# Performance work log

Measured on AMD Instinct MI355X. Metric: run time of the kernel, lower is better.

## Reference

```python
import jax, jax.numpy as jnp
import numpy as np

N = 10000      # nodes
E = 80000      # edges (avg degree 8)
G = 64         # graphs in batch
HID = 256
RBF_K = 16
DEPTH = 6
KA, KC, KE = 16, 6, 5
DE = HID // 3          # 85, per-modality embedding dim
CAT = 3 * HID + RBF_K  # 784, width of [h_i, h_j, rbf, e_emb]
CUTOFF = 10.0


def _gumbel_hard(probs, noise, tau=1.0):
    """F.gumbel_softmax(log(probs), tau, hard=True) with externally supplied gumbel noise."""
    logits = jnp.log(jnp.clip(probs, 1e-12))
    y = jax.nn.softmax((logits + noise) / tau, axis=-1)
    hard = jax.nn.one_hot(jnp.argmax(y, axis=-1), y.shape[-1], dtype=y.dtype)
    return hard + y - jax.lax.stop_gradient(y)  # straight-through


def setup_inputs() -> dict:
    key = jax.random.key(0)
    ks = iter(jax.random.split(key, 80))

    def nrm(shape, fan):
        return jax.random.normal(next(ks), shape, jnp.float32) / np.sqrt(fan).astype(np.float32)

    def gumbel(shape):
        u = jax.random.uniform(next(ks), shape, minval=1e-9, maxval=1.0 - 1e-9)
        return -jnp.log(-jnp.log(u))

    inp = {}
    inp['a_t'] = jax.random.uniform(next(ks), (N, KA))
    inp['c_t'] = jax.random.uniform(next(ks), (N, KC))
    inp['e_t'] = jax.random.uniform(next(ks), (E, KE))
    inp['x_t'] = jax.random.normal(next(ks), (N, 3))
    inp['g_a'] = gumbel((N, KA))
    inp['g_c'] = gumbel((N, KC))
    inp['g_e'] = gumbel((E, KE))

    # embeddings / fuse / lift
    inp['atom_W'] = nrm((KA, DE), KA)
    inp['charge_W'] = nrm((KC, DE), KC)
    inp['bond_W'] = nrm((KE, DE), KE)
    inp['fuse_W'] = nrm((3 * DE, HID), 3 * DE)
    inp['fuse_b'] = jnp.zeros((HID,))
    inp['lift_W'] = nrm((DE, HID), DE)
    inp['lift_b'] = jnp.zeros((HID,))

    # stacked block params (DEPTH blocks)
    inp['phim_W1'] = nrm((DEPTH, CAT, HID), CAT)
    inp['phim_b1'] = jnp.zeros((DEPTH, HID))
    inp['phim_W2'] = nrm((DEPTH, HID, HID), HID)
    inp['phim_b2'] = jnp.zeros((DEPTH, HID))
    inp['phix_W1'] = nrm((DEPTH, HID, HID), HID)
    inp['phix_b1'] = jnp.zeros((DEPTH, HID))
    inp['phix_W2'] = nrm((DEPTH, HID, 1), HID)
    inp['phix_b2'] = jnp.zeros((DEPTH, 1))
    inp['psim_W1'] = nrm((DEPTH, CAT, HID), CAT)
    inp['psim_b1'] = jnp.zeros((DEPTH, HID))
    inp['psim_W2'] = nrm((DEPTH, HID, HID), HID)
    inp['psim_b2'] = jnp.zeros((DEPTH, HID))
    inp['updh_W1'] = nrm((DEPTH, 2 * HID, HID), 2 * HID)
    inp['updh_b1'] = jnp.zeros((DEPTH, HID))
    inp['updh_W2'] = nrm((DEPTH, HID, HID), HID)
    inp['updh_b2'] = jnp.zeros((DEPTH, HID))
    inp['ln_g'] = jnp.ones((DEPTH, HID))
    inp['ln_b'] = jnp.zeros((DEPTH, HID))
    inp['head_W'] = nrm((HID, 1), HID)
    inp['head_b'] = jnp.zeros((1,))

    inp['src'] = jax.random.randint(next(ks), (E,), 0, N)
    inp['dst'] = jax.random.randint(next(ks), (E,), 0, N)
    inp['node_graph'] = jnp.sort(jax.random.randint(next(ks), (N,), 0, G))
    return inp


def reference(a_t, c_t, e_t, x_t, g_a, g_c, g_e,
              atom_W, charge_W, bond_W, fuse_W, fuse_b, lift_W, lift_b,
              phim_W1, phim_b1, phim_W2, phim_b2,
              phix_W1, phix_b1, phix_W2, phix_b2,
              psim_W1, psim_b1, psim_W2, psim_b2,
              updh_W1, updh_b1, updh_W2, updh_b2,
              ln_g, ln_b, head_W, head_b,
              src, dst, node_graph):
    centers = jnp.linspace(0.0, CUTOFF, RBF_K)
    widths = jnp.full((RBF_K,), CUTOFF / RBF_K)

    # encode nodes: gumbel-hard embed atom & charge probs, zero x-slot, fuse
    a_h = _gumbel_hard(a_t, g_a) @ atom_W           # (N, DE)
    c_h = _gumbel_hard(c_t, g_c) @ charge_W         # (N, DE)
    h = jnp.concatenate([a_h, c_h, jnp.zeros_like(a_h)], axis=-1) @ fuse_W + fuse_b  # (N, HID)
    # encode edges
    e_emb = (_gumbel_hard(e_t, g_e) @ bond_W) @ lift_W + lift_b  # (E, HID)

    x = x_t
    for d in range(DEPTH):
        h_i, h_j = h[dst], h[src]                    # gather per edge
        rij = x[dst] - x[src]                        # (E, 3)
        dist = jnp.sqrt(jnp.clip(jnp.sum(rij * rij, -1, keepdims=True), 0.0))
        z = (dist - centers) / (widths + 1e-12)
        rbf = jnp.exp(-0.5 * z * z)                  # (E, RBF_K)
        cat = jnp.concatenate([h_i, h_j, rbf, e_emb], axis=-1)  # (E, 784)
        m = jax.nn.silu(jax.nn.silu(cat @ phim_W1[d] + phim_b1[d]) @ phim_W2[d] + phim_b2[d])
        gate = jax.nn.silu(m @ phix_W1[d] + phix_b1[d]) @ phix_W2[d] + phix_b2[d]  # (E, 1)
        pm = jax.nn.silu(jax.nn.silu(cat @ psim_W1[d] + psim_b1[d]) @ psim_W2[d] + psim_b2[d])
        dx_sum = jax.ops.segment_sum(rij * gate, dst, num_segments=N)   # scatter to dst
        pm_sum = jax.ops.segment_sum(pm, dst, num_segments=N)
        x = x + dx_sum
        u = jax.nn.silu(jnp.concatenate([h, pm_sum], -1) @ updh_W1[d] + updh_b1[d]) @ updh_W2[d] + updh_b2[d]
        z2 = h + u
        mu = jnp.mean(z2, -1, keepdims=True)
        var = jnp.mean((z2 - mu) ** 2, -1, keepdims=True)
        h = (z2 - mu) / jnp.sqrt(var + 1e-5) * ln_g[d] + ln_b[d]

    # mean readout per graph
    cnt = jax.ops.segment_sum(jnp.ones((h.shape[0], 1), h.dtype), node_graph, num_segments=G)
    hg = jax.ops.segment_sum(h, node_graph, num_segments=G) / jnp.maximum(cnt, 1.0)
    out = jax.nn.sigmoid((hg @ head_W + head_b) / 2.0)  # property='score' -> sigmoid, tau=2
    return out
```

## Files before the change

kernel.cpp:

```cpp
#include <hip/hip_runtime.h>
#include <math.h>

#define NN   10000
#define NE   80000
#define NG   64
#define HID  256
#define RBFK 16
#define NDEP 6
#define KA   16
#define KC   6
#define KE   5
#define DE   85
#define CATW 784

typedef __attribute__((ext_vector_type(8))) short bf16x8;
typedef __attribute__((ext_vector_type(4))) float f32x4;
typedef __attribute__((ext_vector_type(2))) __bf16 bf16v2;

#if __has_builtin(__builtin_amdgcn_fdot2_f32_bf16)
#define HAVE_BF16_DOT2 1
#else
#define HAVE_BF16_DOT2 0
#endif

static __device__ __forceinline__ float silu_f(float v) {
  return __fdividef(v, 1.0f + __expf(-v));
}

static __device__ __forceinline__ unsigned short f2bf(float f) {
  union { float f; unsigned int u; } v; v.f = f;
  unsigned int r = v.u + 0x7fff + ((v.u >> 16) & 1);
  return (unsigned short)(r >> 16);
}
static __device__ __forceinline__ float bf2f(unsigned short h) {
  union { unsigned int u; float f; } v; v.u = ((unsigned int)h) << 16;
  return v.f;
}
static __device__ __forceinline__ bf16v2 u2bf2(unsigned int u) {
  union { unsigned int u; bf16v2 v; } x; x.u = u; return x.v;
}

static __device__ __forceinline__ void gload16(const void* g, void* l) {
  __builtin_amdgcn_global_load_lds((const __attribute__((address_space(1))) unsigned int*)g,
                                   (__attribute__((address_space(3))) unsigned int*)l, 16, 0, 0);
}

__global__ void convw_plain(const float* __restrict__ W, unsigned short* __restrict__ Wt, int K,
                            long long wt_dstride, int wt_rowoff) {
  __shared__ float T[32][65];
  int k0 = blockIdx.x * 32, n0 = blockIdx.y * 64, d = blockIdx.z;
  int tid = threadIdx.x;
  int nn = tid & 63, kr = tid >> 6;
  const float* Wd = W + (size_t)d * K * 256;
#pragma unroll
  for (int i = 0; i < 8; ++i) {
    int k = kr + i * 4;
    T[k][nn] = Wd[(size_t)(k0 + k) * 256 + n0 + nn];
  }
  __syncthreads();
  unsigned short* Wtd = Wt + (size_t)d * wt_dstride;
  int kk = tid & 31, nr = tid >> 5;
#pragma unroll
  for (int i = 0; i < 8; ++i) {
    int n = nr + i * 8;
    Wtd[(size_t)(wt_rowoff + n0 + n) * K + k0 + kk] = f2bf(T[kk][n]);
  }
}

__global__ void convw_nodeblk(const float* __restrict__ W, unsigned short* __restrict__ Wt,
                              int src_k0, int nt_base) {
  __shared__ float T[32][65];
  int k0 = blockIdx.x * 32, n0 = blockIdx.y * 64, d = blockIdx.z;
  int tid = threadIdx.x;
  int nn = tid & 63, kr = tid >> 6;
  const float* Wd = W + (size_t)d * CATW * 256;
#pragma unroll
  for (int i = 0; i < 8; ++i) {
    int k = kr + i * 4;
    T[k][nn] = Wd[(size_t)(src_k0 + k0 + k) * 256 + n0 + nn];
  }
  __syncthreads();
  unsigned short* Wtd = Wt + (size_t)d * 1024 * 256;
  int kk = tid & 31, nr = tid >> 5;
#pragma unroll
  for (int i = 0; i < 8; ++i) {
    int n = nr + i * 8;
    Wtd[(size_t)(nt_base + n0 + n) * 256 + k0 + kk] = f2bf(T[kk][n]);
  }
}

__global__ void convw_rbf(const float* __restrict__ phimW1, const float* __restrict__ psimW1,
                          unsigned short* __restrict__ wR) {
  int d = blockIdx.x, j = threadIdx.x;
  int jj = j & 255;
  const float* W = (j < 256) ? phimW1 : psimW1;
  for (int k = 0; k < 16; ++k)
    wR[((size_t)d * 16 + k) * 512 + j] = f2bf(W[(size_t)d * CATW * 256 + (size_t)(512 + k) * 256 + jj]);
}

__global__ void convw_rbf2(const float* __restrict__ phimW1, const float* __restrict__ psimW1,
                           unsigned int* __restrict__ wRp) {
  int d = blockIdx.x, j = threadIdx.x;
  int jj = j & 255;
  const float* W = (j < 256) ? phimW1 : psimW1;
  const float* base = W + (size_t)d * CATW * 256;
  for (int p = 0; p < 8; ++p) {
    unsigned int lo = f2bf(base[(size_t)(512 + 2*p) * 256 + jj]);
    unsigned int hi = f2bf(base[(size_t)(512 + 2*p + 1) * 256 + jj]);
    wRp[((size_t)d * 8 + p) * 512 + j] = lo | (hi << 16);
  }
}

__global__ void tables_kernel(const float* __restrict__ atom_W, const float* __restrict__ charge_W,
                              const float* __restrict__ bond_W, const float* __restrict__ fuse_W,
                              const float* __restrict__ fuse_b, const float* __restrict__ lift_W,
                              const float* __restrict__ lift_b,
                              float* __restrict__ tabA, float* __restrict__ tabC,
                              float* __restrict__ tabEf) {
  int r = blockIdx.x, k = threadIdx.x;
  if (r < KA) {
    float s = 0.f;
    for (int d = 0; d < DE; ++d) s += atom_W[r*DE + d] * fuse_W[d*HID + k];
    tabA[r*HID + k] = s + fuse_b[k];
  } else if (r < KA + KC) {
    int rr = r - KA;
    float s = 0.f;
    for (int d = 0; d < DE; ++d) s += charge_W[rr*DE + d] * fuse_W[(DE + d)*HID + k];
    tabC[rr*HID + k] = s;
  } else {
    int rr = r - KA - KC;
    float s = 0.f;
    for (int d = 0; d < DE; ++d) s += bond_W[rr*DE + d] * lift_W[d*HID + k];
    tabEf[rr*HID + k] = s + lift_b[k];
  }
}

__global__ void tabe1_kernel(const float* __restrict__ tabEf,
                             const float* __restrict__ phimW1, const float* __restrict__ phimb1,
                             const float* __restrict__ psimW1, const float* __restrict__ psimb1,
                             unsigned short* __restrict__ tabE1) {
  int r = blockIdx.x, d = blockIdx.y, j = threadIdx.x;
  const float* W = (j < 256) ? phimW1 : psimW1;
  const float* b = (j < 256) ? phimb1 : psimb1;
  int jj = j & 255;
  float s = b[d*256 + jj];
  for (int k = 0; k < 256; ++k)
    s += tabEf[r*256 + k] * W[(size_t)d*CATW*256 + (size_t)(528 + k)*256 + jj];
  tabE1[((size_t)d*5 + r)*512 + j] = f2bf(s);
}

__global__ void node_init_kernel(const float* __restrict__ a_t, const float* __restrict__ c_t,
                                 const float* __restrict__ g_a, const float* __restrict__ g_c,
                                 const float* __restrict__ x_t, const float* __restrict__ tabA,
                                 const float* __restrict__ tabC, float* __restrict__ h,
                                 unsigned short* __restrict__ hbf, float* __restrict__ x) {
  int n = blockIdx.x;
  __shared__ int s_ia, s_ic;
  if (threadIdx.x == 0) {
    float best = -1e30f; int bi = 0;
    for (int j = 0; j < KA; ++j) {
      float v = logf(fmaxf(a_t[n*KA + j], 1e-12f)) + g_a[n*KA + j];
      if (v > best) { best = v; bi = j; }
    }
    s_ia = bi;
  }
  if (threadIdx.x == 1) {
    float best = -1e30f; int bi = 0;
    for (int j = 0; j < KC; ++j) {
      float v = logf(fmaxf(c_t[n*KC + j], 1e-12f)) + g_c[n*KC + j];
      if (v > best) { best = v; bi = j; }
    }
    s_ic = bi;
  }
  __syncthreads();
  int k = threadIdx.x;
  float v = tabA[s_ia*HID + k] + tabC[s_ic*HID + k];
  h[n*HID + k] = v;
  hbf[n*HID + k] = f2bf(v);
  if (k < 3) x[n*3 + k] = x_t[n*3 + k];
}

__global__ void edge_init_kernel(const float* __restrict__ e_t, const float* __restrict__ g_e,
                                 int* __restrict__ ie) {
  int e = blockIdx.x * blockDim.x + threadIdx.x;
  if (e >= NE) return;
  float best = -1e30f; int bi = 0;
  for (int j = 0; j < KE; ++j) {
    float v = logf(fmaxf(e_t[e*KE + j], 1e-12f)) + g_e[e*KE + j];
    if (v > best) { best = v; bi = j; }
  }
  ie[e] = bi;
}

__global__ void hist_kernel(const int* __restrict__ dst, int* __restrict__ deg) {
  int e = blockIdx.x * 256 + threadIdx.x;
  if (e < NE) atomicAdd(&deg[dst[e]], 1);
}

__global__ void scan_kernel(const int* __restrict__ deg, int* __restrict__ rowstart,
                            int* __restrict__ cursor) {
  __shared__ int tmp[1024];
  int t = threadIdx.x;
  int base = t * 10;
  int local[10];
  int s = 0;
#pragma unroll
  for (int i = 0; i < 10; ++i) { local[i] = deg[base + i]; s += local[i]; }
  tmp[t] = s;
  __syncthreads();
  for (int off = 1; off < 1024; off <<= 1) {
    int v = (t >= off) ? tmp[t - off] : 0;
    __syncthreads();
    tmp[t] += v;
    __syncthreads();
  }
  int run = (t == 0) ? 0 : tmp[t - 1];
#pragma unroll
  for (int i = 0; i < 10; ++i) {
    rowstart[base + i] = run; cursor[base + i] = run; run += local[i];
  }
  if (t == 1023) rowstart[10240] = run;
}

__global__ void fill_kernel(const int* __restrict__ dst, int* __restrict__ cursor,
                            int* __restrict__ eids) {
  int e = blockIdx.x * 256 + threadIdx.x;
  if (e >= NE) return;
  int pos = atomicAdd(&cursor[dst[e]], 1);
  eids[pos] = e;
}

__global__ void sortrows_kernel(const int* __restrict__ rowstart, int* __restrict__ eids) {
  int n = blockIdx.x * 256 + threadIdx.x;
  if (n >= NN) return;
  int s = rowstart[n], e = rowstart[n + 1];
  for (int i = s + 1; i < e; ++i) {
    int v = eids[i]; int j = i - 1;
    while (j >= s && eids[j] > v) { eids[j + 1] = eids[j]; --j; }
    eids[j + 1] = v;
  }
}

__global__ void gbound_kernel(const int* __restrict__ ng, int* __restrict__ gstart) {
  int n = blockIdx.x * 256 + threadIdx.x;
  if (n >= NN) return;
  if (n == 0) {
    for (int g = 0; g <= ng[0]; ++g) gstart[g] = 0;
  } else {
    int a = ng[n-1], b = ng[n];
    for (int g = a + 1; g <= b; ++g) gstart[g] = n;
  }
  if (n == NN - 1) {
    for (int g = ng[n] + 1; g <= NG; ++g) gstart[g] = NN;
  }
}

__global__ __launch_bounds__(256) void combine2_kernel(
    const int* __restrict__ srcp, const int* __restrict__ dstp, const int* __restrict__ iep,
    const float* __restrict__ x,
    const unsigned short* __restrict__ P,
    const unsigned short* __restrict__ tabE1,
    const unsigned short* __restrict__ wR,
    const unsigned int* __restrict__ wRp,
    unsigned short* __restrict__ c1, unsigned short* __restrict__ ps1) {
  const int tid = threadIdx.x;
  const int lane = tid & 63;
  const int e = blockIdx.x * 4 + (tid >> 6);
  const int half = lane >> 5;
  const int c8 = (lane & 31) * 8;
  const int ds = dstp[e], sr = srcp[e], ib = iep[e];
  float r0 = x[ds*3+0] - x[sr*3+0];
  float r1 = x[ds*3+1] - x[sr*3+1];
  float r2 = x[ds*3+2] - x[sr*3+2];
  float dist = sqrtf(r0*r0 + r1*r1 + r2*r2);
  int klo = (int)(dist * 1.5f) - 3;
  klo = klo < 0 ? 0 : (klo > 8 ? 8 : klo);
  const unsigned short* Pb0 = P + (size_t)(half * 2) * NN * 256;
  const unsigned short* Pb1 = P + (size_t)(half * 2 + 1) * NN * 256;
  bf16x8 pa = *(const bf16x8*)&Pb0[(size_t)ds * 256 + c8];
  bf16x8 pb = *(const bf16x8*)&Pb1[(size_t)sr * 256 + c8];
  bf16x8 te = *(const bf16x8*)&tabE1[(size_t)ib * 512 + lane * 8];
  float zv[8];
#pragma unroll
  for (int j = 0; j < 8; ++j)
    zv[j] = bf2f((unsigned short)pa[j]) + bf2f((unsigned short)pb[j]) + bf2f((unsigned short)te[j]);
#if HAVE_BF16_DOT2
  int plo = klo >> 1;
  if (plo > 4) plo = 4;
#pragma unroll
  for (int pp = 0; pp < 4; ++pp) {
    int pr = plo + pp;
    float k0f = (float)(2 * pr);
    float z0 = (dist - 0.66666667f * k0f) * 1.6f;
    float z1 = (dist - 0.66666667f * (k0f + 1.0f)) * 1.6f;
    unsigned int rkp = (unsigned int)f2bf(__expf(-0.5f * z0 * z0)) |
                       ((unsigned int)f2bf(__expf(-0.5f * z1 * z1)) << 16);
    bf16v2 rv = u2bf2(rkp);
    const unsigned int* w8 = wRp + (size_t)pr * 512 + lane * 8;
    uint4 wa = *(const uint4*)w8;
    uint4 wb = *(const uint4*)(w8 + 4);
    zv[0] = __builtin_amdgcn_fdot2_f32_bf16(rv, u2bf2(wa.x), zv[0], false);
    zv[1] = __builtin_amdgcn_fdot2_f32_bf16(rv, u2bf2(wa.y), zv[1], false);
    zv[2] = __builtin_amdgcn_fdot2_f32_bf16(rv, u2bf2(wa.z), zv[2], false);
    zv[3] = __builtin_amdgcn_fdot2_f32_bf16(rv, u2bf2(wa.w), zv[3], false);
    zv[4] = __builtin_amdgcn_fdot2_f32_bf16(rv, u2bf2(wb.x), zv[4], false);
    zv[5] = __builtin_amdgcn_fdot2_f32_bf16(rv, u2bf2(wb.y), zv[5], false);
    zv[6] = __builtin_amdgcn_fdot2_f32_bf16(rv, u2bf2(wb.z), zv[6], false);
    zv[7] = __builtin_amdgcn_fdot2_f32_bf16(rv, u2bf2(wb.w), zv[7], false);
  }
#else
  (void)wRp;
#pragma unroll
  for (int kk = 0; kk < 8; ++kk) {
    int k = klo + kk;
    float z = (dist - 0.66666667f * (float)k) * 1.6f;
    float rk = __expf(-0.5f * z * z);
    bf16x8 wv = *(const bf16x8*)&wR[k * 512 + lane * 8];
#pragma unroll
    for (int j = 0; j < 8; ++j)
      zv[j] += rk * bf2f((unsigned short)wv[j]);
  }
#endif
  unsigned short ov[8];
#pragma unroll
  for (int j = 0; j < 8; ++j) ov[j] = f2bf(silu_f(zv[j]));
  unsigned short* outp = half ? ps1 : c1;
  *(uint4*)&outp[(size_t)e * 256 + c8] = *(uint4*)ov;
}

template<int MODE, bool SILU, bool GATE, bool LNOUT, bool SMALL>
__global__ __launch_bounds__(SMALL ? 256 : 512, 4) void mfma_gemm(
    const unsigned short* __restrict__ A, const unsigned short* __restrict__ A2,
    const unsigned short* __restrict__ Wt,
    const float* __restrict__ bias, const float* __restrict__ bias2,
    unsigned short* __restrict__ C, unsigned short* __restrict__ C2,
    int M, int Kp, int Msplit,
    const float* __restrict__ gw2, float* __restrict__ gout,
    float* __restrict__ hf, unsigned short* __restrict__ hb,
    const float* __restrict__ lng, const float* __restrict__ lnb) {
  constexpr int BM = SMALL ? 64 : 128;
  constexpr int BQ = SMALL ? 8 : 4;
  __shared__ unsigned short lds[SMALL ? 20480 : 24576];
  unsigned short* As = lds;
  unsigned short* Bs = lds + BM * 64;
  const int tid = threadIdx.x;
  const int bn = blockIdx.x * 256;
  const int bm = blockIdx.y * BM;
  const int lane = tid & 63;
  const int w = tid >> 6;
  const int wr = SMALL ? 0 : (w >> 2);
  const int wc = SMALL ? w : (w & 3);
  const int subrow = lane >> 3;
  const int kd = 8 * ((lane & 7) ^ subrow);

  const bool half2 = (MODE == 4) && (bm >= Msplit);
  const unsigned short* Wb = Wt + (half2 ? 256 * 256 : 0);

  unsigned int offB[BQ];
#pragma unroll
  for (int q = 0; q < BQ; ++q)
    offB[q] = (unsigned)(bn + w * (BQ * 8) + q * 8 + subrow) * (unsigned)Kp;

  unsigned int offA[2];
#pragma unroll
  for (int q = 0; q < 2; ++q) {
    int m = bm + w * 16 + q * 8 + subrow;
    int mc = (m < M) ? m : (M - 1);
    offA[q] = (unsigned)mc * 256u;
  }

  const int nt = Kp >> 6;
  f32x4 acc[4][4] = {};

  for (int t = 0; t < nt; ++t) {
    const int k0 = t << 6;
#pragma unroll
    for (int q = 0; q < 2; ++q) {
      const unsigned short* gp;
      if (MODE == 2) gp = (k0 < 256) ? (A + offA[q] + k0 + kd) : (A2 + offA[q] + (k0 - 256) + kd);
      else gp = A + offA[q] + k0 + kd;
      gload16(gp, (char*)As + w * 2048 + q * 1024);
    }
#pragma unroll
    for (int q = 0; q < BQ; ++q)
      gload16(Wb + offB[q] + k0 + kd, (char*)Bs + w * (BQ * 1024) + q * 1024);
    __syncthreads();
#pragma unroll
    for (int ks = 0; ks < 2; ++ks) {
      const int kb = (ks * 64 + ((lane >> 4) << 4)) ^ ((lane & 7) << 4);
      bf16x8 bfv[4];
#pragma unroll
      for (int j = 0; j < 4; ++j)
        bfv[j] = *(const bf16x8*)((const char*)Bs + (wc * 64 + j * 16 + (lane & 15)) * 128 + kb);
#pragma unroll
      for (int i = 0; i < 4; ++i) {
        bf16x8 af = *(const bf16x8*)((const char*)As + (wr * 64 + i * 16 + (lane & 15)) * 128 + kb);
#pragma unroll
        for (int j = 0; j < 4; ++j)
          acc[i][j] = __builtin_amdgcn_mfma_f32_16x16x32_bf16(af, bfv[j], acc[i][j], 0, 0, 0);
      }
    }
    __syncthreads();
  }

  if (GATE) {
    float bcol[4], wcol[4];
#pragma unroll
    for (int j = 0; j < 4; ++j) {
      int col = wc * 64 + j * 16 + (lane & 15);
      bcol[j] = bias[col];
      wcol[j] = gw2[col];
    }
    float* part = (float*)lds;
#pragma unroll
    for (int i = 0; i < 4; ++i) {
#pragma unroll
      for (int q = 0; q < 4; ++q) {
        float lsum = 0.f;
#pragma unroll
        for (int j = 0; j < 4; ++j)
          lsum += silu_f(acc[i][j][q] + bcol[j]) * wcol[j];
        lsum += __shfl_xor(lsum, 1, 64);
        lsum += __shfl_xor(lsum, 2, 64);
        lsum += __shfl_xor(lsum, 4, 64);
        lsum += __shfl_xor(lsum, 8, 64);
        if ((lane & 15) == 0) {
          int rl = wr * 64 + i * 16 + ((lane >> 4) << 2) + q;
          part[wc * BM + rl] = lsum;
        }
      }
    }
    __syncthreads();
    if (tid < BM)
      gout[bm + tid] = part[tid] + part[BM + tid] + part[2*BM + tid] + part[3*BM + tid];
    return;
  }

  if (LNOUT) {
    float bcol[4], lgc[4], lbc[4];
#pragma unroll
    for (int j = 0; j < 4; ++j) {
      int col = wc * 64 + j * 16 + (lane & 15);
      bcol[j] = bias[col]; lgc[j] = lng[col]; lbc[j] = lnb[col];
    }
    float* part = (float*)lds;
    float* stat = part + 4 * BM;
#pragma unroll
    for (int i = 0; i < 4; ++i)
#pragma unroll
      for (int q = 0; q < 4; ++q) {
        int rl = wr * 64 + i * 16 + ((lane >> 4) << 2) + q;
        int grow = bm + rl;
        float s = 0.f;
#pragma unroll
        for (int j = 0; j < 4; ++j) {
          int col = wc * 64 + j * 16 + (lane & 15);
          float hv = (grow < M) ? hf[(size_t)grow * 256 + col] : 0.f;
          float zz = acc[i][j][q] + bcol[j] + hv;
          acc[i][j][q] = zz;
          s += zz;
        }
        s += __shfl_xor(s, 1, 64); s += __shfl_xor(s, 2, 64);
        s += __shfl_xor(s, 4, 64); s += __shfl_xor(s, 8, 64);
        if ((lane & 15) == 0) part[wc * BM + rl] = s;
      }
    __syncthreads();
    if (tid < BM)
      stat[tid] = (part[tid] + part[BM + tid] + part[2*BM + tid] + part[3*BM + tid]) * (1.f / 256.f);
    __syncthreads();
#pragma unroll
    for (int i = 0; i < 4; ++i)
#pragma unroll
      for (int q = 0; q < 4; ++q) {
        int rl = wr * 64 + i * 16 + ((lane >> 4) << 2) + q;
        float mu = stat[rl];
        float s2 = 0.f;
#pragma unroll
        for (int j = 0; j < 4; ++j) { float d_ = acc[i][j][q] - mu; s2 += d_ * d_; }
        s2 += __shfl_xor(s2, 1, 64); s2 += __shfl_xor(s2, 2, 64);
        s2 += __shfl_xor(s2, 4, 64); s2 += __shfl_xor(s2, 8, 64);
        if ((lane & 15) == 0) part[wc * BM + rl] = s2;
      }
    __syncthreads();
    if (tid < BM)
      stat[BM + tid] = 1.f / sqrtf((part[tid] + part[BM + tid] + part[2*BM + tid] + part[3*BM + tid]) * (1.f / 256.f) + 1e-5f);
    __syncthreads();
#pragma unroll
    for (int i = 0; i < 4; ++i)
#pragma unroll
      for (int q = 0; q < 4; ++q) {
        int rl = wr * 64 + i * 16 + ((lane >> 4) << 2) + q;
        int grow = bm + rl;
        if (grow < M) {
          float mu = stat[rl], rs = stat[BM + rl];
#pragma unroll
          for (int j = 0; j < 4; ++j) {
            int col = wc * 64 + j * 16 + (lane & 15);
            float o = (acc[i][j][q] - mu) * rs * lgc[j] + lbc[j];
            hf[(size_t)grow * 256 + col] = o;
            hb[(size_t)grow * 256 + col] = f2bf(o);
          }
        }
      }
    return;
  }

  const float* biasw = bias;
  unsigned short* Cw = C;
  int rowoff = 0;
  if (MODE == 3) Cw = C + (size_t)(bn >> 8) * (size_t)M * 256;
  if (MODE == 4 && half2) { biasw = bias2; Cw = C2; rowoff = Msplit; }

  float bcol[4];
#pragma unroll
  for (int j = 0; j < 4; ++j) bcol[j] = biasw[wc * 64 + j * 16 + (lane & 15)];

  unsigned short* T = lds;
#pragma unroll
  for (int hh = 0; hh < 2; ++hh) {
    if ((wc >> 1) == hh) {
#pragma unroll
      for (int i = 0; i < 4; ++i)
#pragma unroll
        for (int j = 0; j < 4; ++j)
#pragma unroll
          for (int q = 0; q < 4; ++q) {
            int rl = wr * 64 + i * 16 + ((lane >> 4) << 2) + q;
            int cl = (wc & 1) * 64 + j * 16 + (lane & 15);
            float v = acc[i][j][q] + bcol[j];
            if (SILU) v = silu_f(v);
            T[rl * 136 + cl] = f2bf(v);
          }
    }
    __syncthreads();
#pragma unroll
    for (int it = 0; it < 4; ++it) {
      int row = it * (BM / 4) + (tid >> 4);
      int grow = bm + row;
      if (grow < M) {
        uint4 v = *(const uint4*)&T[row * 136 + (tid & 15) * 8];
        *(uint4*)&Cw[(size_t)(grow - rowoff) * 256 + hh * 128 + (tid & 15) * 8] = v;
      }
    }
    __syncthreads();
  }
}

__global__ __launch_bounds__(256, 2) void upd_fused_kernel(
    const unsigned short* __restrict__ hbf, const unsigned short* __restrict__ pmbf,
    const unsigned short* __restrict__ W1t,
    const unsigned short* __restrict__ W2t,
    const float* __restrict__ b1, const float* __restrict__ b2,
    float* __restrict__ hf, unsigned short* __restrict__ hb,
    const float* __restrict__ lng, const float* __restrict__ lnb, int M) {
  __shared__ unsigned short lds[16384 + 16896];
  unsigned short* Bs = lds;
  unsigned short* As = lds + 16384;
  unsigned short* T  = lds + 16384;
  const int tid = threadIdx.x;
  const int bm = blockIdx.y * 64;
  const int lane = tid & 63;
  const int w = tid >> 6;
  const int subrow = lane >> 3;
  const int kd = 8 * ((lane & 7) ^ subrow);

  unsigned int offA[2];
#pragma unroll
  for (int q = 0; q < 2; ++q) {
    int m = bm + w * 16 + q * 8 + subrow;
    int mc = (m < M) ? m : (M - 1);
    offA[q] = (unsigned)mc * 256u;
  }
  unsigned int offB1[8];
#pragma unroll
  for (int q = 0; q < 8; ++q)
    offB1[q] = (unsigned)(w * 64 + q * 8 + subrow) * 512u;

  f32x4 acc[4][4] = {};
  for (int t = 0; t < 8; ++t) {
    const int k0 = t << 6;
#pragma unroll
    for (int q = 0; q < 2; ++q) {
      const unsigned short* gp = (k0 < 256) ? (hbf + offA[q] + k0 + kd)
                                            : (pmbf + offA[q] + (k0 - 256) + kd);
      gload16(gp, (char*)As + w * 2048 + q * 1024);
    }
#pragma unroll
    for (int q = 0; q < 8; ++q)
      gload16(W1t + offB1[q] + k0 + kd, (char*)Bs + w * 8192 + q * 1024);
    __syncthreads();
#pragma unroll
    for (int ks = 0; ks < 2; ++ks) {
      const int kb = (ks * 64 + ((lane >> 4) << 4)) ^ ((lane & 7) << 4);
      bf16x8 bfv[4];
#pragma unroll
      for (int j = 0; j < 4; ++j)
        bfv[j] = *(const bf16x8*)((const char*)Bs + (w * 64 + j * 16 + (lane & 15)) * 128 + kb);
#pragma unroll
      for (int i = 0; i < 4; ++i) {
        bf16x8 af = *(const bf16x8*)((const char*)As + (i * 16 + (lane & 15)) * 128 + kb);
#pragma unroll
        for (int j = 0; j < 4; ++j)
          acc[i][j] = __builtin_amdgcn_mfma_f32_16x16x32_bf16(af, bfv[j], acc[i][j], 0, 0, 0);
      }
    }
    __syncthreads();
  }

  {
    float bcol[4];
#pragma unroll
    for (int j = 0; j < 4; ++j) bcol[j] = b1[w * 64 + j * 16 + (lane & 15)];
#pragma unroll
    for (int i = 0; i < 4; ++i)
#pragma unroll
      for (int j = 0; j < 4; ++j)
#pragma unroll
        for (int q = 0; q < 4; ++q) {
          int rl = i * 16 + ((lane >> 4) << 2) + q;
          int cl = w * 64 + j * 16 + (lane & 15);
          T[rl * 264 + cl] = f2bf(silu_f(acc[i][j][q] + bcol[j]));
        }
  }
  __syncthreads();

  unsigned int offB2[8];
#pragma unroll
  for (int q = 0; q < 8; ++q)
    offB2[q] = (unsigned)(w * 64 + q * 8 + subrow) * 256u;

  f32x4 acc2[4][4] = {};
  for (int t = 0; t < 4; ++t) {
    const int k0 = t << 6;
#pragma unroll
    for (int q = 0; q < 8; ++q)
      gload16(W2t + offB2[q] + k0 + kd, (char*)Bs + w * 8192 + q * 1024);
    __syncthreads();
#pragma unroll
    for (int ks = 0; ks < 2; ++ks) {
      const int kb = (ks * 64 + ((lane >> 4) << 4)) ^ ((lane & 7) << 4);
      const int ka = k0 + ks * 32 + ((lane >> 4) << 3);
      bf16x8 bfv[4];
#pragma unroll
      for (int j = 0; j < 4; ++j)
        bfv[j] = *(const bf16x8*)((const char*)Bs + (w * 64 + j * 16 + (lane & 15)) * 128 + kb);
#pragma unroll
      for (int i = 0; i < 4; ++i) {
        bf16x8 af = *(const bf16x8*)&T[(i * 16 + (lane & 15)) * 264 + ka];
#pragma unroll
        for (int j = 0; j < 4; ++j)
          acc2[i][j] = __builtin_amdgcn_mfma_f32_16x16x32_bf16(af, bfv[j], acc2[i][j], 0, 0, 0);
      }
    }
    __syncthreads();
  }

  {
    float bcol[4], lgc[4], lbc[4];
#pragma unroll
    for (int j = 0; j < 4; ++j) {
      int col = w * 64 + j * 16 + (lane & 15);
      bcol[j] = b2[col]; lgc[j] = lng[col]; lbc[j] = lnb[col];
    }
    float* part = (float*)lds;
    float* stat = part + 256;
#pragma unroll
    for (int i = 0; i < 4; ++i)
#pragma unroll
      for (int q = 0; q < 4; ++q) {
        int rl = i * 16 + ((lane >> 4) << 2) + q;
        int grow = bm + rl;
        float s = 0.f;
#pragma unroll
        for (int j = 0; j < 4; ++j) {
          int col = w * 64 + j * 16 + (lane & 15);
          float hv = (grow < M) ? hf[(size_t)grow * 256 + col] : 0.f;
          float zz = acc2[i][j][q] + bcol[j] + hv;
          acc2[i][j][q] = zz;
          s += zz;
        }
        s += __shfl_xor(s, 1, 64); s += __shfl_xor(s, 2, 64);
        s += __shfl_xor(s, 4, 64); s += __shfl_xor(s, 8, 64);
        if ((lane & 15) == 0) part[w * 64 + rl] = s;
      }
    __syncthreads();
    if (tid < 64)
      stat[tid] = (part[tid] + part[64 + tid] + part[128 + tid] + part[192 + tid]) * (1.f / 256.f);
    __syncthreads();
#pragma unroll
    for (int i = 0; i < 4; ++i)
#pragma unroll
      for (int q = 0; q < 4; ++q) {
        int rl = i * 16 + ((lane >> 4) << 2) + q;
        float mu = stat[rl];
        float s2 = 0.f;
#pragma unroll
        for (int j = 0; j < 4; ++j) { float d_ = acc2[i][j][q] - mu; s2 += d_ * d_; }
        s2 += __shfl_xor(s2, 1, 64); s2 += __shfl_xor(s2, 2, 64);
        s2 += __shfl_xor(s2, 4, 64); s2 += __shfl_xor(s2, 8, 64);
        if ((lane & 15) == 0) part[w * 64 + rl] = s2;
      }
    __syncthreads();
    if (tid < 64)
      stat[64 + tid] = 1.f / sqrtf((part[tid] + part[64 + tid] + part[128 + tid] + part[192 + tid]) * (1.f / 256.f) + 1e-5f);
    __syncthreads();
#pragma unroll
    for (int i = 0; i < 4; ++i)
#pragma unroll
      for (int q = 0; q < 4; ++q) {
        int rl = i * 16 + ((lane >> 4) << 2) + q;
        int grow = bm + rl;
        if (grow < M) {
          float mu = stat[rl], rs = stat[64 + rl];
#pragma unroll
          for (int j = 0; j < 4; ++j) {
            int col = w * 64 + j * 16 + (lane & 15);
            float o = (acc2[i][j][q] - mu) * rs * lgc[j] + lbc[j];
            hf[(size_t)grow * 256 + col] = o;
            hb[(size_t)grow * 256 + col] = f2bf(o);
          }
        }
      }
  }
}

__global__ void gather_pm_dx(const unsigned short* __restrict__ pm, const float* __restrict__ gate,
                             const float* __restrict__ xcur, const int* __restrict__ srcp,
                             const int* __restrict__ rowstart, const int* __restrict__ eids,
                             const float* __restrict__ gb2,
                             unsigned short* __restrict__ pmbf, float* __restrict__ xnxt) {
  int n = blockIdx.x, k = threadIdx.x;
  int s = rowstart[n], e1 = rowstart[n + 1];
  float acc = 0.f, dx = 0.f;
  float b2 = gb2[0];
  float xn = (k < 3) ? xcur[n*3 + k] : 0.f;
  for (int t = s; t < e1; ++t) {
    int e = eids[t];
    acc += bf2f(pm[(size_t)e*HID + k]);
    if (k < 3) dx += (xn - xcur[srcp[e]*3 + k]) * (gate[e] + b2);
  }
  pmbf[(size_t)n*HID + k] = f2bf(acc);
  if (k < 3) xnxt[n*3 + k] = xn + dx;
}

__global__ void readout_kernel(const float* __restrict__ h, const int* __restrict__ gstart,
                               const float* __restrict__ head_W, const float* __restrict__ head_b,
                               float* __restrict__ out) {
  int g = blockIdx.x, k = threadIdx.x;
  int s = gstart[g], e = gstart[g + 1];
  float acc = 0.f;
  for (int n = s; n < e; ++n) acc += h[(size_t)n * HID + k];
  float v = acc * head_W[k];
  __shared__ float red[4];
  int lane = k & 63, wv = k >> 6;
#pragma unroll
  for (int off = 32; off > 0; off >>= 1) v += __shfl_down(v, off, 64);
  if (lane == 0) red[wv] = v;
  __syncthreads();
  if (k == 0) {
    float dot = red[0] + red[1] + red[2] + red[3];
    float c = fmaxf((float)(e - s), 1.0f);
    float val = (dot / c + head_b[0]) * 0.5f;
    out[g] = __fdividef(1.0f, 1.0f + __expf(-val));
  }
}

extern "C" void kernel_launch(void* const* d_in, const int* in_sizes, int n_in,
                              void* d_out, int out_size, void* d_ws, size_t ws_size,
                              hipStream_t stream) {
  (void)in_sizes; (void)n_in; (void)out_size; (void)ws_size;
  const float* a_t      = (const float*)d_in[0];
  const float* c_t      = (const float*)d_in[1];
  const float* e_t      = (const float*)d_in[2];
  const float* x_t      = (const float*)d_in[3];
  const float* g_a      = (const float*)d_in[4];
  const float* g_c      = (const float*)d_in[5];
  const float* g_e      = (const float*)d_in[6];
  const float* atom_W   = (const float*)d_in[7];
  const float* charge_W = (const float*)d_in[8];
  const float* bond_W   = (const float*)d_in[9];
  const float* fuse_W   = (const float*)d_in[10];
  const float* fuse_b   = (const float*)d_in[11];
  const float* lift_W   = (const float*)d_in[12];
  const float* lift_b   = (const float*)d_in[13];
  const float* phim_W1  = (const float*)d_in[14];
  const float* phim_b1  = (const float*)d_in[15];
  const float* phim_W2  = (const float*)d_in[16];
  const float* phim_b2  = (const float*)d_in[17];
  const float* phix_W1  = (const float*)d_in[18];
  const float* phix_b1  = (const float*)d_in[19];
  const float* phix_W2  = (const float*)d_in[20];
  const float* phix_b2  = (const float*)d_in[21];
  const float* psim_W1  = (const float*)d_in[22];
  const float* psim_b1  = (const float*)d_in[23];
  const float* psim_W2  = (const float*)d_in[24];
  const float* psim_b2  = (const float*)d_in[25];
  const float* updh_W1  = (const float*)d_in[26];
  const float* updh_b1  = (const float*)d_in[27];
  const float* updh_W2  = (const float*)d_in[28];
  const float* updh_b2  = (const float*)d_in[29];
  const float* ln_g     = (const float*)d_in[30];
  const float* ln_b     = (const float*)d_in[31];
  const float* head_W   = (const float*)d_in[32];
  const float* head_b   = (const float*)d_in[33];
  const int*   src      = (const int*)d_in[34];
  const int*   dst      = (const int*)d_in[35];
  const int*   ngraph   = (const int*)d_in[36];
  float* out = (float*)d_out;

  char* p = (char*)d_ws;
  auto carve = [&](size_t bytes) -> char* {
    char* r = p; p += (bytes + 255) & ~(size_t)255; return r;
  };
  float*          h     = (float*)carve((size_t)NN*HID*4);
  unsigned short* hbf   = (unsigned short*)carve((size_t)NN*HID*2);
  float*          xposA = (float*)carve((size_t)NN*3*4);
  float*          xposB = (float*)carve((size_t)NN*3*4);
  int*            ie    = (int*)carve((size_t)NE*4);
  float*          tabA  = (float*)carve((size_t)KA*HID*4);
  float*          tabC  = (float*)carve((size_t)KC*HID*4);
  float*          tabEf = (float*)carve((size_t)KE*HID*4);
  float*          gate  = (float*)carve((size_t)NE*4);
  unsigned short* pmbf  = (unsigned short*)carve((size_t)NN*HID*2);
  float*          zbias = (float*)carve(256*4);
  unsigned short* buf01 = (unsigned short*)carve((size_t)2*NE*HID*2);
  unsigned short* bufM  = (unsigned short*)carve((size_t)NE*HID*2);
  unsigned short* bufPM = (unsigned short*)carve((size_t)NE*HID*2);
  unsigned short* P     = (unsigned short*)carve((size_t)4*NN*HID*2);
  int* deg      = (int*)carve(10240*4);
  int* cursor   = (int*)carve(10240*4);
  int* rowstart = (int*)carve(10241*4);
  int* eids     = (int*)carve((size_t)NE*4);
  int* gstart   = (int*)carve((NG+1)*4);
  unsigned short* wNode  = (unsigned short*)carve((size_t)NDEP*1024*256*2);
  unsigned short* wMPM   = (unsigned short*)carve((size_t)NDEP*512*256*2);
  unsigned short* wPhix1 = (unsigned short*)carve((size_t)NDEP*256*256*2);
  unsigned short* wUpd1  = (unsigned short*)carve((size_t)NDEP*256*512*2);
  unsigned short* wUpd2  = (unsigned short*)carve((size_t)NDEP*256*256*2);
  unsigned short* wRbf   = (unsigned short*)carve((size_t)NDEP*16*512*2);
  unsigned int*   wRbfP  = (unsigned int*)carve((size_t)NDEP*8*512*4);
  unsigned short* tabE1  = (unsigned short*)carve((size_t)NDEP*5*512*2);

  unsigned short* c1buf = buf01;
  unsigned short* psbuf = buf01 + (size_t)NE*HID;

  convw_nodeblk<<<dim3(8,4,NDEP), 256, 0, stream>>>(phim_W1, wNode, 0,   0);
  convw_nodeblk<<<dim3(8,4,NDEP), 256, 0, stream>>>(phim_W1, wNode, 256, 256);
  convw_nodeblk<<<dim3(8,4,NDEP), 256, 0, stream>>>(psim_W1, wNode, 0,   512);
  convw_nodeblk<<<dim3(8,4,NDEP), 256, 0, stream>>>(psim_W1, wNode, 256, 768);
  convw_plain<<<dim3(8,4,NDEP), 256, 0, stream>>>(phim_W2, wMPM, 256, 512*256, 0);
  convw_plain<<<dim3(8,4,NDEP), 256, 0, stream>>>(psim_W2, wMPM, 256, 512*256, 256);
  convw_plain<<<dim3(8,4,NDEP), 256, 0, stream>>>(phix_W1, wPhix1, 256, 256*256, 0);
  convw_plain<<<dim3(8,4,NDEP), 256, 0, stream>>>(updh_W2, wUpd2, 256, 256*256, 0);
  convw_plain<<<dim3(16,4,NDEP), 256, 0, stream>>>(updh_W1, wUpd1, 512, 256*512, 0);
  convw_rbf<<<NDEP, 512, 0, stream>>>(phim_W1, psim_W1, wRbf);
  convw_rbf2<<<NDEP, 512, 0, stream>>>(phim_W1, psim_W1, wRbfP);
  hipMemsetAsync(zbias, 0, 256*4, stream);

  tables_kernel<<<KA + KC + KE, 256, 0, stream>>>(atom_W, charge_W, bond_W, fuse_W, fuse_b,
                                                  lift_W, lift_b, tabA, tabC, tabEf);
  tabe1_kernel<<<dim3(5, NDEP), 512, 0, stream>>>(tabEf, phim_W1, phim_b1, psim_W1, psim_b1, tabE1);
  node_init_kernel<<<NN, 256, 0, stream>>>(a_t, c_t, g_a, g_c, x_t, tabA, tabC, h, hbf, xposA);
  edge_init_kernel<<<(NE + 255)/256, 256, 0, stream>>>(e_t, g_e, ie);

  hipMemsetAsync(deg, 0, 10240*4, stream);
  hist_kernel<<<(NE + 255)/256, 256, 0, stream>>>(dst, deg);
  scan_kernel<<<1, 1024, 0, stream>>>(deg, rowstart, cursor);
  fill_kernel<<<(NE + 255)/256, 256, 0, stream>>>(dst, cursor, eids);
  sortrows_kernel<<<(NN + 255)/256, 256, 0, stream>>>(rowstart, eids);
  gbound_kernel<<<(NN + 255)/256, 256, 0, stream>>>(ngraph, gstart);

  dim3 gridP(4, (NN + 63)/64);
  dim3 gridE(1, NE/128);
  dim3 gridE2(1, 2*NE/128);
  dim3 gridNU(1, (NN + 63)/64);

  float* xcur = xposA;
  float* xnxt = xposB;

  for (int d = 0; d < NDEP; ++d) {
    const float* pb2m = phim_b2 + (size_t)d*HID;
    const float* pxb1 = phix_b1 + (size_t)d*HID;
    const float* pxW2 = phix_W2 + (size_t)d*HID;
    const float* pxb2 = phix_b2 + (size_t)d;
    const float* psb2 = psim_b2 + (size_t)d*HID;
    const float* pub1 = updh_b1 + (size_t)d*HID;
    const float* pub2 = updh_b2 + (size_t)d*HID;

    mfma_gemm<3, false, false, false, true><<<gridP, 256, 0, stream>>>(
        hbf, nullptr, wNode + (size_t)d*1024*256, zbias, nullptr, P, nullptr, NN, 256, 0,
        nullptr, nullptr, nullptr, nullptr, nullptr, nullptr);
    combine2_kernel<<<NE/4, 256, 0, stream>>>(
        src, dst, ie, xcur, P, tabE1 + (size_t)d*5*512, wRbf + (size_t)d*16*512,
        wRbfP + (size_t)d*8*512, c1buf, psbuf);
    mfma_gemm<4, true, false, false, false><<<gridE2, 512, 0, stream>>>(
        buf01, nullptr, wMPM + (size_t)d*512*256, pb2m, psb2, bufM, bufPM, 2*NE, 256, NE,
        nullptr, nullptr, nullptr, nullptr, nullptr, nullptr);
    mfma_gemm<0, false, true, false, false><<<gridE, 512, 0, stream>>>(
        bufM, nullptr, wPhix1 + (size_t)d*256*256, pxb1, nullptr, nullptr, nullptr, NE, 256, 0,
        pxW2, gate, nullptr, nullptr, nullptr, nullptr);
    gather_pm_dx<<<NN, 256, 0, stream>>>(bufPM, gate, xcur, src, rowstart, eids, pxb2, pmbf, xnxt);
    upd_fused_kernel<<<gridNU, 256, 0, stream>>>(
        hbf, pmbf, wUpd1 + (size_t)d*256*512, wUpd2 + (size_t)d*256*256,
        pub1, pub2, h, hbf, ln_g + (size_t)d*HID, ln_b + (size_t)d*HID, NN);

    float* tmp = xcur; xcur = xnxt; xnxt = tmp;
  }

  readout_kernel<<<NG, 256, 0, stream>>>(h, gstart, head_W, head_b, out);
}
```

Baseline: 1.374 ms.

## Fuse phim second layer with phix gate MLP into one edge kernel

Splits the combined phim/psim second-layer GEMM so that psim runs alone, and adds a new kernel that chains the phim second layer (with SiLU) and the phix first layer plus the dot product with phix_W2 to produce the per-edge gate directly. The intermediate m tensor (E x 256 bf16) stays in LDS instead of being written to and reread from global memory, and the bufM buffer is dropped. In exchange, the new kernel uses 64-row tiles with 256 threads and reloads weights per tile, which may reduce GEMM efficiency compared with the batched 2E-row launch.

Measured after the change: 1.395 ms. No clear change (+1.5%).

```diff
diff --git a/kernel.cpp b/kernel.cpp
--- a/kernel.cpp
+++ b/kernel.cpp
@@ -546,10 +546,146 @@
   }
 }
 
+__global__ __launch_bounds__(256, 2) void mgate_kernel(
+    const unsigned short* __restrict__ c1,
+    const unsigned short* __restrict__ W2mt,
+    const unsigned short* __restrict__ Wx1t,
+    const float* __restrict__ b2m, const float* __restrict__ bx1,
+    const float* __restrict__ wx2,
+    float* __restrict__ gate, int M) {
+  __shared__ unsigned short lds[16384 + 16896];
+  unsigned short* Bs = lds;
+  unsigned short* As = lds + 16384;
+  unsigned short* T  = lds + 16384;
+  const int tid = threadIdx.x;
+  const int bm = blockIdx.y * 64;
+  const int lane = tid & 63;
+  const int w = tid >> 6;
+  const int subrow = lane >> 3;
+  const int kd = 8 * ((lane & 7) ^ subrow);
+
+  unsigned int offA[2];
+#pragma unroll
+  for (int q = 0; q < 2; ++q) {
+    int m = bm + w * 16 + q * 8 + subrow;
+    int mc = (m < M) ? m : (M - 1);
+    offA[q] = (unsigned)mc * 256u;
+  }
+  unsigned int offB[8];
+#pragma unroll
+  for (int q = 0; q < 8; ++q)
+    offB[q] = (unsigned)(w * 64 + q * 8 + subrow) * 256u;
+
+  f32x4 acc[4][4] = {};
+  for (int t = 0; t < 4; ++t) {
+    const int k0 = t << 6;
+#pragma unroll
+    for (int q = 0; q < 2; ++q)
+      gload16(c1 + offA[q] + k0 + kd, (char*)As + w * 2048 + q * 1024);
+#pragma unroll
+    for (int q = 0; q < 8; ++q)
+      gload16(W2mt + offB[q] + k0 + kd, (char*)Bs + w * 8192 + q * 1024);
+    __syncthreads();
+#pragma unroll
+    for (int ks = 0; ks < 2; ++ks) {
+      const int kb = (ks * 64 + ((lane >> 4) << 4)) ^ ((lane & 7) << 4);
+      bf16x8 bfv[4];
+#pragma unroll
+      for (int j = 0; j < 4; ++j)
+        bfv[j] = *(const bf16x8*)((const char*)Bs + (w * 64 + j * 16 + (lane & 15)) * 128 + kb);
+#pragma unroll
+      for (int i = 0; i < 4; ++i) {
+        bf16x8 af = *(const bf16x8*)((const char*)As + (i * 16 + (lane & 15)) * 128 + kb);
+#pragma unroll
+        for (int j = 0; j < 4; ++j)
+          acc[i][j] = __builtin_amdgcn_mfma_f32_16x16x32_bf16(af, bfv[j], acc[i][j], 0, 0, 0);
+      }
+    }
+    __syncthreads();
+  }
+
+  {
+    float bcol[4];
+#pragma unroll
+    for (int j = 0; j < 4; ++j) bcol[j] = b2m[w * 64 + j * 16 + (lane & 15)];
+#pragma unroll
+    for (int i = 0; i < 4; ++i)
+#pragma unroll
+      for (int j = 0; j < 4; ++j)
+#pragma unroll
+        for (int q = 0; q < 4; ++q) {
+          int rl = i * 16 + ((lane >> 4) << 2) + q;
+          int cl = w * 64 + j * 16 + (lane & 15);
+          T[rl * 264 + cl] = f2bf(silu_f(acc[i][j][q] + bcol[j]));
+        }
+  }
+  __syncthreads();
+
+  f32x4 acc2[4][4] = {};
+  for (int t = 0; t < 4; ++t) {
+    const int k0 = t << 6;
+#pragma unroll
+    for (int q = 0; q < 8; ++q)
+      gload16(Wx1t + offB[q] + k0 + kd, (char*)Bs + w * 8192 + q * 1024);
+    __syncthreads();
+#pragma unroll
+    for (int ks = 0; ks < 2; ++ks) {
+      const int kb = (ks * 64 + ((lane >> 4) << 4)) ^ ((lane & 7) << 4);
+      const int ka = k0 + ks * 32 + ((lane >> 4) << 3);
+      bf16x8 bfv[4];
+#pragma unroll
+      for (int j = 0; j < 4; ++j)
+        bfv[j] = *(const bf16x8*)((const char*)Bs + (w * 64 + j * 16 + (lane & 15)) * 128 + kb);
+#pragma unroll
+      for (int i = 0; i < 4; ++i) {
+        bf16x8 af = *(const bf16x8*)&T[(i * 16 + (lane & 15)) * 264 + ka];
+#pragma unroll
+        for (int j = 0; j < 4; ++j)
+          acc2[i][j] = __builtin_amdgcn_mfma_f32_16x16x32_bf16(af, bfv[j], acc2[i][j], 0, 0, 0);
+      }
+    }
+    __syncthreads();
+  }
+
+  {
+    float bcol[4], wcol[4];
+#pragma unroll
+    for (int j = 0; j < 4; ++j) {
+      int col = w * 64 + j * 16 + (lane & 15);
+      bcol[j] = bx1[col];
+      wcol[j] = wx2[col];
+    }
+    float* part = (float*)lds;
+#pragma unroll
+    for (int i = 0; i < 4; ++i) {
+#pragma unroll
+      for (int q = 0; q < 4; ++q) {
+        float lsum = 0.f;
+#pragma unroll
+        for (int j = 0; j < 4; ++j)
+          lsum += silu_f(acc2[i][j][q] + bcol[j]) * wcol[j];
+        lsum += __shfl_xor(lsum, 1, 64);
+        lsum += __shfl_xor(lsum, 2, 64);
+        lsum += __shfl_xor(lsum, 4, 64);
+        lsum += __shfl_xor(lsum, 8, 64);
+        if ((lane & 15) == 0) {
+          int rl = i * 16 + ((lane >> 4) << 2) + q;
+          part[w * 64 + rl] = lsum;
+        }
+      }
+    }
+    __syncthreads();
+    if (tid < 64) {
+      int grow = bm + tid;
+      if (grow < M)
+        gate[grow] = part[tid] + part[64 + tid] + part[128 + tid] + part[192 + tid];
+    }
+  }
+}
+
 __global__ __launch_bounds__(256, 2) void upd_fused_kernel(
     const unsigned short* __restrict__ hbf, const unsigned short* __restrict__ pmbf,
-    const unsigned short* __restrict__ W1t,
-    const unsigned short* __restrict__ W2t,
+    const unsigned short* __restrict__ W1t, const unsigned short* __restrict__ W2t,
     const float* __restrict__ b1, const float* __restrict__ b2,
     float* __restrict__ hf, unsigned short* __restrict__ hb,
     const float* __restrict__ lng, const float* __restrict__ lnb, int M) {
@@ -824,7 +960,6 @@
   unsigned short* pmbf  = (unsigned short*)carve((size_t)NN*HID*2);
   float*          zbias = (float*)carve(256*4);
   unsigned short* buf01 = (unsigned short*)carve((size_t)2*NE*HID*2);
-  unsigned short* bufM  = (unsigned short*)carve((size_t)NE*HID*2);
   unsigned short* bufPM = (unsigned short*)carve((size_t)NE*HID*2);
   unsigned short* P     = (unsigned short*)carve((size_t)4*NN*HID*2);
   int* deg      = (int*)carve(10240*4);
@@ -872,7 +1007,7 @@
 
   dim3 gridP(4, (NN + 63)/64);
   dim3 gridE(1, NE/128);
-  dim3 gridE2(1, 2*NE/128);
+  dim3 gridMG(1, (NE + 63)/64);
   dim3 gridNU(1, (NN + 63)/64);
 
   float* xcur = xposA;
@@ -893,12 +1028,12 @@
     combine2_kernel<<<NE/4, 256, 0, stream>>>(
         src, dst, ie, xcur, P, tabE1 + (size_t)d*5*512, wRbf + (size_t)d*16*512,
         wRbfP + (size_t)d*8*512, c1buf, psbuf);
-    mfma_gemm<4, true, false, false, false><<<gridE2, 512, 0, stream>>>(
-        buf01, nullptr, wMPM + (size_t)d*512*256, pb2m, psb2, bufM, bufPM, 2*NE, 256, NE,
+    mfma_gemm<0, true, false, false, false><<<gridE, 512, 0, stream>>>(
+        psbuf, nullptr, wMPM + (size_t)d*512*256 + 256*256, psb2, nullptr, bufPM, nullptr, NE, 256, 0,
         nullptr, nullptr, nullptr, nullptr, nullptr, nullptr);
-    mfma_gemm<0, false, true, false, false><<<gridE, 512, 0, stream>>>(
-        bufM, nullptr, wPhix1 + (size_t)d*256*256, pxb1, nullptr, nullptr, nullptr, NE, 256, 0,
-        pxW2, gate, nullptr, nullptr, nullptr, nullptr);
+    mgate_kernel<<<gridMG, 256, 0, stream>>>(
+        c1buf, wMPM + (size_t)d*512*256, wPhix1 + (size_t)d*256*256,
+        pb2m, pxb1, pxW2, gate, NE);
     gather_pm_dx<<<NN, 256, 0, stream>>>(bufPM, gate, xcur, src, rowstart, eids, pxb2, pmbf, xnxt);
     upd_fused_kernel<<<gridNU, 256, 0, stream>>>(
         hbf, pmbf, wUpd1 + (size_t)d*256*512, wUpd2 + (size_t)d*256*256,
```
